# Optimization experiments

Hardware: AMD Instinct MI355X
Metric: run time of the kernel (lower is better)

Reference implementation:

```python
import jax, jax.numpy as jnp
import numpy as np

C = 32
SHIFTS = (1, 2, 4)
KSIZE = 4  # trans_layer: kernel KSIZE+1, stride KSIZE, pad KSIZE//2
EPS_NORM = 1e-12
EPS_BN = 1e-5


def _make_diff_kernels(c):
    # 8 fixed 3x3 difference kernels, tiled per channel for depthwise conv.
    d1 = np.array([[[-1, 0, 0], [0, 1, 0], [0, 0, 0]],
                   [[0, -1, 0], [0, 1, 0], [0, 0, 0]],
                   [[0, 0, -1], [0, 1, 0], [0, 0, 0]],
                   [[0, 0, 0], [0, 1, -1], [0, 0, 0]]], dtype=np.float32)
    d1 = d1.reshape(4, 1, 3, 3)
    d2 = d1[:, :, ::-1, ::-1].copy()
    delta = np.concatenate([d1, d2], axis=0)          # [8,1,3,3]
    return jnp.asarray(np.tile(delta, (c, 1, 1, 1)))  # [8C,1,3,3]


DIFF_KERNELS = _make_diff_kernels(C)


def conv2d(x, w, stride=1, pad=0, dilation=1, groups=1):
    return jax.lax.conv_general_dilated(
        x, w, (stride, stride), [(pad, pad), (pad, pad)],
        rhs_dilation=(dilation, dilation),
        dimension_numbers=('NCHW', 'OIHW', 'NCHW'),
        feature_group_count=groups)


def l2norm(x, axis=-1):
    n = jnp.sqrt(jnp.sum(x * x, axis=axis, keepdims=True))
    return x / jnp.maximum(n, EPS_NORM)


def setup_inputs() -> dict:
    key = jax.random.key(0)
    ks = jax.random.split(key, 8)
    S = len(SHIFTS)
    return {
        'cen': jax.random.normal(ks[0], (2, C, 256, 256), jnp.float32),
        'trans_W': jax.random.normal(ks[1], (C, C, 5, 5), jnp.float32) * 0.05,
        'trans_b': jax.random.normal(ks[2], (C,), jnp.float32) * 0.05,
        'query_W': jax.random.normal(ks[3], (C, C, 1, 1), jnp.float32) * 0.05,
        'value_W': jax.random.normal(ks[4], (S, C, C, 1, 1), jnp.float32) * 0.05,
        'key_W': jax.random.normal(ks[5], (S, C, C, 1, 1), jnp.float32) * 0.05,
        'out_W': jax.random.normal(ks[6], (C, C, 1, 1), jnp.float32) * 0.05,
        'bn_gamma': jnp.ones((C,), jnp.float32),
        'bn_beta': jnp.zeros((C,), jnp.float32),
        'bn_mean': jnp.zeros((C,), jnp.float32),
        'bn_var': jnp.ones((C,), jnp.float32),
    }


def reference(cen, trans_W, trans_b, query_W, value_W, key_W, out_W,
              bn_gamma, bn_beta, bn_mean, bn_var):
    b, _, w, h = cen.shape
    S = len(SHIFTS)
    size = (w * h) // (KSIZE * KSIZE)

    # trans_layer: kernel KSIZE+1, stride KSIZE, pad KSIZE//2
    kv_cen = conv2d(cen, trans_W, stride=KSIZE, pad=KSIZE // 2) \
        + trans_b[None, :, None, None]

    keys, values = [], []
    for i, d in enumerate(SHIFTS):
        v = conv2d(cen, value_W[i])          # [b,C,w,h]
        k = conv2d(kv_cen, key_W[i])         # [b,C,w',h']
        # depthwise dilated difference conv -> 8 outputs per channel
        v = conv2d(v, DIFF_KERNELS, pad=d, dilation=d, groups=C)  # [b,8C,w,h]
        k = conv2d(k, DIFF_KERNELS, pad=d, dilation=d, groups=C)  # [b,8C,w',h']
        keys.append(k)
        values.append(v)

    querys = conv2d(kv_cen, query_W)  # [b,C,w',h']

    keys = jnp.stack(keys, axis=2).reshape(b, C, 8 * S, size)       # [b,C,8S,size]
    values = jnp.stack(values, axis=2).reshape(b, C, 8 * S, w * h)  # [b,C,8S,wh]

    keys = jnp.swapaxes(l2norm(keys, -1), -2, -1)        # [b,C,size,8S]
    querys = l2norm(querys.reshape(b, C, 1, size), -1)   # [b,C,1,size]

    score = jnp.matmul(querys, keys)   # [b,C,1,8S]  cosine sims
    score = l2norm(score, -1)
    out = jnp.matmul(score, values).reshape(b, C, w, h)

    # out_conv: 1x1 conv -> BN (eval mode, running stats) -> ReLU
    out = conv2d(out, out_W)
    inv = jax.lax.rsqrt(bn_var + EPS_BN)
    out = (out - bn_mean[None, :, None, None]) * (bn_gamma * inv)[None, :, None, None] \
        + bn_beta[None, :, None, None]
    return jax.nn.relu(out)
```

## Files before the change

kernel.cpp:

```cpp
#include <hip/hip_runtime.h>
#include <hip/hip_bf16.h>


#define CC 32
#define HW 256
#define KVW 64

__global__ __launch_bounds__(256, 2) void k1_trans(const float* __restrict__ cen,
                                                   const float* __restrict__ tW,
                                                   const float* __restrict__ tB,
                                                   float* __restrict__ kv) {
  __shared__ alignas(16) float part[2][2][64];
  int bid = blockIdx.x;
  int b = bid >> 9, cog = (bid >> 6) & 7, y = bid & 63;
  int tid = threadIdx.x;
  int x = tid & 63;
  int w = __builtin_amdgcn_readfirstlane(tid >> 6);
  int copair = w >> 1;
  int cihalf = w & 1;
  int co0 = cog * 4 + copair * 2;
  int ci0 = cihalf * 16;

  float acc0 = 0.f, acc1 = 0.f;
  const float4 z4 = {0.f, 0.f, 0.f, 0.f};

  int roff[5];
  bool rok[5];
#pragma unroll
  for (int r = 0; r < 5; r++) {
    int row = 4 * y - 2 + r;
    rok[r] = (row >= 0);
    roff[r] = (row < 0 ? 0 : row) * HW;
  }

  for (int cc4 = 0; cc4 < 16; cc4 += 4) {
    int ci = ci0 + cc4;
    const float* pc[4];
#pragma unroll
    for (int c = 0; c < 4; c++) pc[c] = cen + (size_t)(b * CC + ci + c) * 65536 + 4 * x;
    float4 A[4][5], B[4][5];
#pragma unroll
    for (int c = 0; c < 4; c++) {
#pragma unroll
      for (int r = 0; r < 5; r++) {
        A[c][r] = (x > 0) ? *(const float4*)(pc[c] + roff[r] - 4) : z4;
        B[c][r] = *(const float4*)(pc[c] + roff[r]);
      }
    }
#pragma unroll
    for (int r = 0; r < 5; r++) {
      if (!rok[r]) continue;
#pragma unroll
      for (int c = 0; c < 4; c++) {
        const float* wa = tW + (co0 * CC + ci + c) * 25 + r * 5;
        const float* wb = wa + CC * 25;
        acc0 += wa[0] * A[c][r].z + wa[1] * A[c][r].w + wa[2] * B[c][r].x +
                wa[3] * B[c][r].y + wa[4] * B[c][r].z;
        acc1 += wb[0] * A[c][r].z + wb[1] * A[c][r].w + wb[2] * B[c][r].x +
                wb[3] * B[c][r].y + wb[4] * B[c][r].z;
      }
    }
  }

  if (cihalf == 1) {
    part[copair][0][x] = acc0;
    part[copair][1][x] = acc1;
  }
  __syncthreads();
  if (cihalf == 0) {
    acc0 += part[copair][0][x];
    acc1 += part[copair][1][x];
    kv[((b * CC + co0) * KVW + y) * KVW + x] = acc0 + tB[co0];
    kv[((b * CC + co0 + 1) * KVW + y) * KVW + x] = acc1 + tB[co0 + 1];
  }
}

__device__ inline float wred64(float v) {
#pragma unroll
  for (int off = 1; off < 64; off <<= 1) v += __shfl_xor(v, off);
  return v;
}

__global__ __launch_bounds__(1024) void k2i_partial(const float* __restrict__ kv,
                                                    const float* __restrict__ qW,
                                                    const float* __restrict__ kW,
                                                    float* __restrict__ pars) {
  __shared__ alignas(16) float kl[4096];
  __shared__ float wredl[16][18];
  int bid = blockIdx.x;
  int bc = bid / 3, i = bid - bc * 3;
  int b = bc >> 5, c = bc & 31;
  int tid = threadIdx.x;
  int lane = tid & 63, w = tid >> 6;
  int xx = tid & 63;
  int ybase = tid >> 6;

  float qreg[4];
#pragma unroll
  for (int r = 0; r < 4; r++) {
    int px = r * 1024 + tid;
    float q = 0.f, kk = 0.f;
    for (int ci = 0; ci < CC; ci++) {
      float val = kv[(b * CC + ci) * 4096 + px];
      q += qW[c * CC + ci] * val;
      kk += kW[(i * CC + c) * CC + ci] * val;
    }
    qreg[r] = q;
    kl[px] = kk;
  }
  __syncthreads();

  float q2 = 0.f;
#pragma unroll
  for (int r = 0; r < 4; r++) q2 += qreg[r] * qreg[r];
  q2 = wred64(q2);
  if (lane == 0) wredl[w][16] = q2;

  constexpr int DYt[8] = {-1, -1, -1, 0, 1, 1, 1, 0};
  constexpr int DXt[8] = {-1, 0, 1, 1, 1, 0, -1, -1};
  const int d = 1 << i;
#pragma unroll
  for (int n = 0; n < 8; n++) {
    const int dy = DYt[n], dx = DXt[n];
    int xn = xx + dx * d;
    bool xok = (xn >= 0 && xn < KVW);
    float dacc = 0.f, macc = 0.f;
#pragma unroll
    for (int r = 0; r < 4; r++) {
      int yy = r * 16 + ybase;
      int px = yy * KVW + xx;
      float kc = kl[px];
      int yn = yy + dy * d;
      float kn = (xok && yn >= 0 && yn < KVW) ? kl[yn * KVW + xn] : 0.f;
      float df = kc - kn;
      dacc += qreg[r] * df;
      macc += df * df;
    }
    dacc = wred64(dacc);
    macc = wred64(macc);
    if (lane == 0) {
      wredl[w][n] = dacc;
      wredl[w][8 + n] = macc;
    }
  }
  __syncthreads();

  float* pp = pars + (size_t)bid * 32;
  if (tid < 8) {
    float D = 0.f, M = 0.f;
    for (int w2 = 0; w2 < 16; w2++) {
      D += wredl[w2][tid];
      M += wredl[w2][8 + tid];
    }
    pp[tid] = D;
    pp[8 + tid] = M;
  }
  if (tid == 0) {
    float Q = 0.f;
    for (int w2 = 0; w2 < 16; w2++) Q += wredl[w2][16];
    pp[16] = Q;
  }
}

__global__ __launch_bounds__(64) void k2f_finalize(const float* __restrict__ pars,
                                                   float* __restrict__ scores) {
  __shared__ float srl[24];
  int bc = blockIdx.x;
  int t = threadIdx.x;
  if (t < 24) {
    int i = t >> 3, n = t & 7;
    const float* pp = pars + (size_t)(bc * 3 + i) * 32;
    float D = pp[n];
    float M = pp[8 + n];
    float Q = pars[(size_t)(bc * 3) * 32 + 16];
    float sr = D / (fmaxf(sqrtf(M), 1e-12f) * fmaxf(sqrtf(Q), 1e-12f));
    srl[t] = sr;
  }
  __syncthreads();
  if (t < 24) {
    float r2 = 0.f;
    for (int j = 0; j < 24; j++) r2 += srl[j] * srl[j];
    scores[bc * 24 + t] = srl[t] / fmaxf(sqrtf(r2), 1e-12f);
  }
}

__global__ __launch_bounds__(256) void k3a_values(const float* __restrict__ cen,
                                                  const float* __restrict__ vW,
                                                  __hip_bfloat16* __restrict__ v) {
  int bid = blockIdx.x;
  int b = bid >> 9, blk = bid & 511;
  int tid = threadIdx.x;
  int lane = tid & 63;
  int cg = __builtin_amdgcn_readfirstlane(tid >> 6);
  int px = blk * 128 + lane * 2;

  float2 cr[CC];
#pragma unroll
  for (int ci = 0; ci < CC; ci++)
    cr[ci] = *(const float2*)(cen + (size_t)(b * CC + ci) * 65536 + px);

#pragma unroll
  for (int i = 0; i < 3; i++) {
#pragma unroll
    for (int cc = 0; cc < 8; cc++) {
      int c = cg * 8 + cc;
      const float* wp = vW + (i * CC + c) * CC;
      float a0 = 0.f, a1 = 0.f;
#pragma unroll
      for (int ci = 0; ci < CC; ci++) {
        a0 += wp[ci] * cr[ci].x;
        a1 += wp[ci] * cr[ci].y;
      }
      __hip_bfloat16 h0 = __float2bfloat16(a0);
      __hip_bfloat16 h1 = __float2bfloat16(a1);
      unsigned int pk = (unsigned int)(*(unsigned short*)&h0) |
                        ((unsigned int)(*(unsigned short*)&h1) << 16);
      *(unsigned int*)((unsigned short*)v + (((size_t)((i * 2 + b) * CC + c)) << 16) +
                       px) = pk;
    }
  }
}

__global__ __launch_bounds__(256) void k3b_combine(const __hip_bfloat16* __restrict__ v,
                                                   const float* __restrict__ scores,
                                                   const float* __restrict__ oW,
                                                   const float* __restrict__ gamma,
                                                   const float* __restrict__ beta,
                                                   const float* __restrict__ mean,
                                                   const float* __restrict__ var,
                                                   float* __restrict__ out) {
  __shared__ alignas(16) float vt[3 * 24 * 24 * 4];
  __shared__ alignas(16) float sl[27][32];
  __shared__ alignas(16) float owl[32][32];
  __shared__ float bns[32], bnb[32];

  int bid = blockIdx.x;
  int b = bid >> 8, tile = bid & 255;
  int ty = tile >> 4, tx = tile & 15;
  int tid = threadIdx.x;
  int ly = tid >> 4, lx = tid & 15;

  for (int f = tid; f < 24 * 32; f += 256) {
    int j = f >> 5, c = f & 31;
    sl[j][c] = scores[(b * CC + c) * 24 + j];
  }
  for (int f = tid; f < 1024; f += 256) owl[f >> 5][f & 31] = oW[f];
  if (tid < 32) {
    float inv = rsqrtf(var[tid] + 1e-5f);
    float sc = gamma[tid] * inv;
    bns[tid] = sc;
    bnb[tid] = beta[tid] - mean[tid] * sc;
  }
  __syncthreads();
  if (tid < 32) {
#pragma unroll
    for (int i = 0; i < 3; i++) {
      float s = 0.f;
      for (int n = 0; n < 8; n++) s += sl[i * 8 + n][tid];
      sl[24 + i][tid] = s;
    }
  }

  int ldsoff[4], pxoff[4], ibase[4];
  bool okp[4];
#pragma unroll
  for (int it = 0; it < 4; it++) {
    int p = tid + it * 256;
    bool act = (p < 864);
    int pp = act ? p : 0;
    int i = pp / 288;
    int rem = pp - i * 288;
    int r = rem / 12;
    int col = (rem - r * 12) * 2;
    int gy = ty * 16 + r - 4, gx = tx * 16 + col - 4;
    okp[it] = act && gy >= 0 && gy < HW && gx >= 0 && gx < HW;
    pxoff[it] = gy * HW + gx;
    ibase[it] = (i * 2 + b) * CC;
    ldsoff[it] = ((i * 24 + r) * 24 + col) * 4;
  }

  constexpr int DYt[8] = {-1, -1, -1, 0, 1, 1, 1, 0};
  constexpr int DXt[8] = {-1, 0, 1, 1, 1, 0, -1, -1};

  float acc[32];
#pragma unroll
  for (int co = 0; co < 32; co++) acc[co] = 0.f;

  unsigned int pf[4][4];
  const unsigned short* vs = (const unsigned short*)v;

#pragma unroll
  for (int it = 0; it < 4; it++)
#pragma unroll
    for (int cp = 0; cp < 4; cp++)
      pf[it][cp] = okp[it]
                       ? *(const unsigned int*)(vs + (((size_t)(ibase[it] + cp)) << 16) +
                                                pxoff[it])
                       : 0u;

  for (int cg = 0; cg < 8; cg++) {
    __syncthreads();
#pragma unroll
    for (int it = 0; it < 4; it++) {
      if (it == 3 && tid >= 96) continue;
      float4 lo, hi;
      lo.x = __uint_as_float(pf[it][0] << 16);
      lo.y = __uint_as_float(pf[it][1] << 16);
      lo.z = __uint_as_float(pf[it][2] << 16);
      lo.w = __uint_as_float(pf[it][3] << 16);
      hi.x = __uint_as_float(pf[it][0] & 0xffff0000u);
      hi.y = __uint_as_float(pf[it][1] & 0xffff0000u);
      hi.z = __uint_as_float(pf[it][2] & 0xffff0000u);
      hi.w = __uint_as_float(pf[it][3] & 0xffff0000u);
      *(float4*)&vt[ldsoff[it]] = lo;
      *(float4*)&vt[ldsoff[it] + 4] = hi;
    }
    if (cg < 7) {
      int cb = (cg + 1) * 4;
#pragma unroll
      for (int it = 0; it < 4; it++)
#pragma unroll
        for (int cp = 0; cp < 4; cp++)
          pf[it][cp] = okp[it] ? *(const unsigned int*)(vs +
                                                        (((size_t)(ibase[it] + cb + cp))
                                                         << 16) +
                                                        pxoff[it])
                               : 0u;
    }
    __syncthreads();

    float4 pre = {0.f, 0.f, 0.f, 0.f};
#pragma unroll
    for (int i = 0; i < 3; i++) {
      const int d = 1 << i;
      float4 S4 = *(const float4*)&sl[24 + i][cg * 4];
      float4 ctr = *(const float4*)&vt[((i * 24 + (ly + 4)) * 24 + (lx + 4)) * 4];
      pre.x += S4.x * ctr.x;
      pre.y += S4.y * ctr.y;
      pre.z += S4.z * ctr.z;
      pre.w += S4.w * ctr.w;
#pragma unroll
      for (int n = 0; n < 8; n++) {
        float4 sj = *(const float4*)&sl[i * 8 + n][cg * 4];
        float4 nb = *(const float4*)&vt[((i * 24 + (ly + 4 + DYt[n] * d)) * 24 +
                                         (lx + 4 + DXt[n] * d)) * 4];
        pre.x -= sj.x * nb.x;
        pre.y -= sj.y * nb.y;
        pre.z -= sj.z * nb.z;
        pre.w -= sj.w * nb.w;
      }
    }
#pragma unroll
    for (int co = 0; co < 32; co++) {
      float4 ow = *(const float4*)&owl[co][cg * 4];
      acc[co] += ow.x * pre.x + ow.y * pre.y + ow.z * pre.z + ow.w * pre.w;
    }
  }

  int gy = ty * 16 + ly, gx = tx * 16 + lx;
#pragma unroll
  for (int co = 0; co < 32; co++) {
    float val = acc[co] * bns[co] + bnb[co];
    out[((size_t)(b * CC + co) << 16) + gy * HW + gx] = fmaxf(val, 0.f);
  }
}

extern "C" void kernel_launch(void* const* d_in, const int* in_sizes, int n_in,
                              void* d_out, int out_size, void* d_ws, size_t ws_size,
                              hipStream_t stream) {
  const float* cen = (const float*)d_in[0];
  const float* trans_W = (const float*)d_in[1];
  const float* trans_b = (const float*)d_in[2];
  const float* query_W = (const float*)d_in[3];
  const float* value_W = (const float*)d_in[4];
  const float* key_W = (const float*)d_in[5];
  const float* out_W = (const float*)d_in[6];
  const float* bn_gamma = (const float*)d_in[7];
  const float* bn_beta = (const float*)d_in[8];
  const float* bn_mean = (const float*)d_in[9];
  const float* bn_var = (const float*)d_in[10];
  float* out = (float*)d_out;

  float* kv = (float*)d_ws;
  float* scores = (float*)((char*)d_ws + 524288);
  __hip_bfloat16* v = (__hip_bfloat16*)((char*)d_ws + 532480);
  float* pars = (float*)((char*)d_ws + 25673728);

  k1_trans<<<1024, 256, 0, stream>>>(cen, trans_W, trans_b, kv);
  k2i_partial<<<192, 1024, 0, stream>>>(kv, query_W, key_W, pars);
  k2f_finalize<<<64, 64, 0, stream>>>(pars, scores);
  k3a_values<<<1024, 256, 0, stream>>>(cen, value_W, v);
  k3b_combine<<<512, 256, 0, stream>>>(v, scores, out_W, bn_gamma, bn_beta, bn_mean,
                                       bn_var, out);
}
```

Measured before the change: 172.8 us.

## Restructure strided 5x5 conv to compute 16 output channels per thread with 8-way input split

The trans conv kernel now has each thread accumulate 16 output channels over 4 input channels. Each block of 512 threads covers one row and half the output channels, with the 8 waves splitting the input channels and reducing through shared memory. Each input tile is loaded once per block instead of once per group of 2 output channels, which cuts redundant global reads of cen by about 8x. Block indices are also remapped for locality. In exchange the kernel needs 16 accumulators per thread, a 32KB shared buffer and a larger reduction, and it launches only 256 blocks, which may lower occupancy.

```diff
diff --git a/kernel.cpp b/kernel.cpp
--- a/kernel.cpp
+++ b/kernel.cpp
@@ -6,23 +6,23 @@
 #define HW 256
 #define KVW 64
 
-__global__ __launch_bounds__(256, 2) void k1_trans(const float* __restrict__ cen,
+__global__ __launch_bounds__(512, 2) void k1_trans(const float* __restrict__ cen,
                                                    const float* __restrict__ tW,
                                                    const float* __restrict__ tB,
                                                    float* __restrict__ kv) {
-  __shared__ alignas(16) float part[2][2][64];
-  int bid = blockIdx.x;
-  int b = bid >> 9, cog = (bid >> 6) & 7, y = bid & 63;
+  __shared__ alignas(16) float part[8][16][64];
+  int bid0 = blockIdx.x;
+  int bid = (bid0 & 7) * 32 + (bid0 >> 3);
+  int b = bid >> 7, y = (bid >> 1) & 63, coh = bid & 1;
   int tid = threadIdx.x;
   int x = tid & 63;
   int w = __builtin_amdgcn_readfirstlane(tid >> 6);
-  int copair = w >> 1;
-  int cihalf = w & 1;
-  int co0 = cog * 4 + copair * 2;
-  int ci0 = cihalf * 16;
-
-  float acc0 = 0.f, acc1 = 0.f;
-  const float4 z4 = {0.f, 0.f, 0.f, 0.f};
+  int ci0 = w * 4;
+  int co0 = coh * 16;
+
+  float acc[16];
+#pragma unroll
+  for (int co = 0; co < 16; co++) acc[co] = 0.f;
 
   int roff[5];
   bool rok[5];
@@ -33,45 +33,42 @@
     roff[r] = (row < 0 ? 0 : row) * HW;
   }
 
-  for (int cc4 = 0; cc4 < 16; cc4 += 4) {
-    int ci = ci0 + cc4;
-    const float* pc[4];
-#pragma unroll
-    for (int c = 0; c < 4; c++) pc[c] = cen + (size_t)(b * CC + ci + c) * 65536 + 4 * x;
-    float4 A[4][5], B[4][5];
-#pragma unroll
-    for (int c = 0; c < 4; c++) {
+  const float4 z4 = {0.f, 0.f, 0.f, 0.f};
+
+#pragma unroll
+  for (int cc = 0; cc < 4; cc++) {
+    int ci = ci0 + cc;
+    const float* pc = cen + (size_t)(b * CC + ci) * 65536 + 4 * x;
+    float4 A[5], B[5];
+#pragma unroll
+    for (int r = 0; r < 5; r++) {
+      A[r] = (rok[r] && x > 0) ? *(const float4*)(pc + roff[r] - 4) : z4;
+      B[r] = rok[r] ? *(const float4*)(pc + roff[r]) : z4;
+    }
+#pragma unroll
+    for (int co = 0; co < 16; co++) {
+      const float* wp = tW + ((co0 + co) * CC + ci) * 25;
 #pragma unroll
       for (int r = 0; r < 5; r++) {
-        A[c][r] = (x > 0) ? *(const float4*)(pc[c] + roff[r] - 4) : z4;
-        B[c][r] = *(const float4*)(pc[c] + roff[r]);
+        acc[co] += wp[r * 5 + 0] * A[r].z + wp[r * 5 + 1] * A[r].w +
+                   wp[r * 5 + 2] * B[r].x + wp[r * 5 + 3] * B[r].y +
+                   wp[r * 5 + 4] * B[r].z;
       }
     }
-#pragma unroll
-    for (int r = 0; r < 5; r++) {
-      if (!rok[r]) continue;
-#pragma unroll
-      for (int c = 0; c < 4; c++) {
-        const float* wa = tW + (co0 * CC + ci + c) * 25 + r * 5;
-        const float* wb = wa + CC * 25;
-        acc0 += wa[0] * A[c][r].z + wa[1] * A[c][r].w + wa[2] * B[c][r].x +
-                wa[3] * B[c][r].y + wa[4] * B[c][r].z;
-        acc1 += wb[0] * A[c][r].z + wb[1] * A[c][r].w + wb[2] * B[c][r].x +
-                wb[3] * B[c][r].y + wb[4] * B[c][r].z;
-      }
-    }
-  }
-
-  if (cihalf == 1) {
-    part[copair][0][x] = acc0;
-    part[copair][1][x] = acc1;
-  }
-  __syncthreads();
-  if (cihalf == 0) {
-    acc0 += part[copair][0][x];
-    acc1 += part[copair][1][x];
-    kv[((b * CC + co0) * KVW + y) * KVW + x] = acc0 + tB[co0];
-    kv[((b * CC + co0 + 1) * KVW + y) * KVW + x] = acc1 + tB[co0 + 1];
+  }
+
+#pragma unroll
+  for (int co = 0; co < 16; co++) part[w][co][x] = acc[co];
+  __syncthreads();
+
+#pragma unroll
+  for (int k = 0; k < 2; k++) {
+    int o = tid + k * 512;
+    int co = o >> 6, xx = o & 63;
+    float s = 0.f;
+#pragma unroll
+    for (int ww = 0; ww < 8; ww++) s += part[ww][co][xx];
+    kv[((b * CC + co0 + co) * KVW + y) * KVW + xx] = s + tB[co0 + co];
   }
 }
 
@@ -386,7 +383,7 @@
   __hip_bfloat16* v = (__hip_bfloat16*)((char*)d_ws + 532480);
   float* pars = (float*)((char*)d_ws + 25673728);
 
-  k1_trans<<<1024, 256, 0, stream>>>(cen, trans_W, trans_b, kv);
+  k1_trans<<<256, 512, 0, stream>>>(cen, trans_W, trans_b, kv);
   k2i_partial<<<192, 1024, 0, stream>>>(kv, query_W, key_W, pars);
   k2f_finalize<<<64, 64, 0, stream>>>(pars, scores);
   k3a_values<<<1024, 256, 0, stream>>>(cen, value_W, v);
```

After: 186.1 us. 1.08x slower.
